# Kernel tuning notes

Hardware: AMD Instinct MI355X
Metric: run time of the kernel (lower is better)

## Reference

```python
import jax, jax.numpy as jnp
import numpy as np

N = 32          # agents_num
IN_DIM = 16     # node feature dim (excluding 2 pos cols)
HID = 128
HEADS = 4
OUT = 5
DUEL_H = 256
RADIUS = 0.3
LATENT = HID + HID * HEADS * 2  # 1152
BS = 128


def _lin(k, i, o):
    s = 1.0 / np.sqrt(i)
    return jax.random.uniform(k, (i, o), minval=-s, maxval=s, dtype=jnp.float32)


def setup_inputs() -> dict:
    key = jax.random.key(0)
    ks = jax.random.split(key, 16)
    pos = jax.random.uniform(ks[0], (BS, N, 2))
    feats = jax.random.normal(ks[1], (BS, N, IN_DIM))
    aidx = jax.random.randint(ks[2], (BS,), 0, N).astype(jnp.float32)
    node = jnp.concatenate([pos, feats], axis=-1).reshape(BS, N * (2 + IN_DIM))
    obs = jnp.concatenate([node, aidx[:, None]], axis=1)  # (BS, N*(2+IN_DIM)+1)
    return {
        "obs": obs,
        "enc_w1": _lin(ks[3], IN_DIM, HID), "enc_b1": jnp.zeros((HID,)),
        "enc_w2": _lin(ks[4], HID, HID), "enc_b2": jnp.zeros((HID,)),
        "wl1": _lin(ks[5], HID, HEADS * HID), "wr1": _lin(ks[6], HID, HEADS * HID),
        "att1": jax.random.normal(ks[7], (HEADS, HID)) * 0.1, "bias1": jnp.zeros((HEADS * HID,)),
        "wl2": _lin(ks[8], HID * HEADS, HEADS * HID), "wr2": _lin(ks[9], HID * HEADS, HEADS * HID),
        "att2": jax.random.normal(ks[10], (HEADS, HID)) * 0.1, "bias2": jnp.zeros((HEADS * HID,)),
        "q_w1": _lin(ks[11], LATENT, DUEL_H), "q_b1": jnp.zeros((DUEL_H,)),
        "q_w2": _lin(ks[12], DUEL_H, OUT), "q_b2": jnp.zeros((OUT,)),
        "v_w1": _lin(ks[13], LATENT, DUEL_H), "v_b1": jnp.zeros((DUEL_H,)),
        "v_w2": _lin(ks[14], DUEL_H, 1), "v_b2": jnp.zeros((1,)),
    }


def _gatv2(x, adj, wl, wr, att, bias):
    # Dense-masked GATv2 (PyG semantics: lin_l on source j, lin_r on target i,
    # leaky_relu(x_i + x_j) . att, softmax over neighbors j, aggregate lin_l(x_j)).
    bs, n, _ = x.shape
    gl = (x @ wl).reshape(bs, n, HEADS, HID)  # source transform
    gr = (x @ wr).reshape(bs, n, HEADS, HID)  # target transform
    e = jax.nn.leaky_relu(gr[:, :, None] + gl[:, None, :], 0.2)  # [b, i, j, h, c]
    logits = jnp.einsum('bijhc,hc->bijh', e, att)
    logits = jnp.where(adj[..., None], logits, -jnp.inf)  # diag always True (self loops)
    alpha = jax.nn.softmax(logits, axis=2)
    out = jnp.einsum('bijh,bjhc->bihc', alpha, gl).reshape(bs, n, HEADS * HID)
    return out + bias


def reference(obs, enc_w1, enc_b1, enc_w2, enc_b2,
              wl1, wr1, att1, bias1, wl2, wr2, att2, bias2,
              q_w1, q_b1, q_w2, q_b2, v_w1, v_b1, v_w2, v_b2):
    bs = obs.shape[0]
    node = obs[:, :-1].reshape(bs, N, 2 + IN_DIM)
    pos, feats = node[..., :2], node[..., 2:]
    aidx = jnp.clip(obs[:, -1], 0, N - 1).astype(jnp.int32)

    # radius_graph (per-graph, loop=False) + GATv2 add_self_loops => diag True
    d2 = jnp.sum((pos[:, :, None] - pos[:, None, :]) ** 2, axis=-1)  # [bs, N, N]
    adj = (d2 < RADIUS ** 2) | jnp.eye(N, dtype=bool)

    # encoder MLP then ReLU (as in forward)
    h = jax.nn.relu(feats @ enc_w1 + enc_b1)
    x = jax.nn.relu(h @ enc_w2 + enc_b2)  # [bs, N, HID]

    b = jnp.arange(bs)
    x1 = x[b, aidx]  # [bs, HID]

    x = jax.nn.relu(_gatv2(x, adj, wl1, wr1, att1, bias1))  # [bs, N, HID*HEADS]
    x2 = x[b, aidx]

    x = jax.nn.relu(_gatv2(x, adj, wl2, wr2, att2, bias2))
    x3 = x[b, aidx]

    x_cat = jnp.concatenate([x1, x2, x3], axis=1)  # [bs, LATENT]

    q = jax.nn.relu(x_cat @ q_w1 + q_b1) @ q_w2 + q_b2  # [bs, OUT]
    v = jax.nn.relu(x_cat @ v_w1 + v_b1) @ v_w2 + v_b2  # [bs, 1]
    return q - q.mean(axis=1, keepdims=True) + v
```

## Files before the change

kernel.cpp:

```cpp
#include <hip/hip_runtime.h>
#include <hip/hip_bf16.h>

typedef unsigned int uint_t;
typedef unsigned short ushort_t;
typedef __attribute__((ext_vector_type(8))) short short8;
typedef __attribute__((ext_vector_type(4))) float floatx4;

__device__ __forceinline__ float4 fma4(float4 a, float s, float4 w){
  a.x += s*w.x; a.y += s*w.y; a.z += s*w.z; a.w += s*w.w; return a;
}
__device__ __forceinline__ float4 relu4(float4 a){
  return make_float4(fmaxf(a.x,0.f),fmaxf(a.y,0.f),fmaxf(a.z,0.f),fmaxf(a.w,0.f));
}
__device__ __forceinline__ unsigned bf16rne(float f){
  unsigned u = __float_as_uint(f);
  return (u + 0x7fffu + ((u>>16)&1u)) >> 16;
}
__device__ __forceinline__ uint_t packbf(float f){
  unsigned hb = bf16rne(f);
  float hf = __uint_as_float(hb<<16);
  unsigned lb = bf16rne(f - hf);
  return (hb<<16) | lb;
}
__device__ __forceinline__ uint4 pack4(float4 v){
  uint4 u; u.x=packbf(v.x); u.y=packbf(v.y); u.z=packbf(v.z); u.w=packbf(v.w); return u;
}
__device__ __forceinline__ float unpk(uint_t u){
  return __uint_as_float(u & 0xffff0000u) + __uint_as_float(u<<16);
}
#define UNPACK8(u0,u1,hi,lo) \
  hi[0]=(short)(u0.x>>16); lo[0]=(short)u0.x; \
  hi[1]=(short)(u0.y>>16); lo[1]=(short)u0.y; \
  hi[2]=(short)(u0.z>>16); lo[2]=(short)u0.z; \
  hi[3]=(short)(u0.w>>16); lo[3]=(short)u0.w; \
  hi[4]=(short)(u1.x>>16); lo[4]=(short)u1.x; \
  hi[5]=(short)(u1.y>>16); lo[5]=(short)u1.y; \
  hi[6]=(short)(u1.z>>16); lo[6]=(short)u1.z; \
  hi[7]=(short)(u1.w>>16); lo[7]=(short)u1.w;


template<int NKC>
__device__ __forceinline__ void hgemm_body(
    const uint_t* __restrict__ xcatpk,
    const ushort_t* __restrict__ qw1Thi, const ushort_t* __restrict__ qw1Tlo,
    const ushort_t* __restrict__ vw1Thi, const ushort_t* __restrict__ vw1Tlo,
    float* __restrict__ part, int ks, int ct, int t, int k0c, int slot0)
{
  const int w = t>>6, lane = t&63, m = lane&15, quad = lane>>4;
  const ushort_t* Bhi = (ct<4) ? qw1Thi : vw1Thi;
  const int cbl = (ct<4) ? ct*64 : (ct-4)*64;
  const int cbg = (ct<4) ? ct*64 : 256 + (ct-4)*64;
  const int kb = k0c + ks*NKC;
  const uint_t* ap = xcatpk + (size_t)w*18432 + m*32 + quad*8 + (size_t)kb*512;
  const ushort_t* bp0 = Bhi + (size_t)((cbl>>4)+0)*18432 + m*32 + quad*8 + (size_t)kb*512;
  const ushort_t* bp1 = Bhi + (size_t)((cbl>>4)+1)*18432 + m*32 + quad*8 + (size_t)kb*512;
  const ushort_t* bp2 = Bhi + (size_t)((cbl>>4)+2)*18432 + m*32 + quad*8 + (size_t)kb*512;
  const ushort_t* bp3 = Bhi + (size_t)((cbl>>4)+3)*18432 + m*32 + quad*8 + (size_t)kb*512;
  const size_t lod = (size_t)(qw1Tlo - qw1Thi);
  floatx4 acc[4];
  #pragma unroll
  for (int i=0;i<4;i++) acc[i] = (floatx4){0.f,0.f,0.f,0.f};
  #pragma unroll
  for (int kc=0; kc<NKC; kc++){
    const uint4 ua0 = *(const uint4*)(ap);
    const uint4 ua1 = *(const uint4*)(ap+4);
    ap += 512;
    short8 ahi, alo;
    UNPACK8(ua0,ua1,ahi,alo)
    const ushort_t* bps[4] = {bp0, bp1, bp2, bp3};
    #pragma unroll
    for (int nt=0; nt<4; nt++){
      const short8 bh = *(const short8*)(bps[nt] + kc*512);
      const short8 bl = *(const short8*)(bps[nt] + kc*512 + lod);
      acc[nt] = __builtin_amdgcn_mfma_f32_16x16x32_bf16(ahi, bh, acc[nt], 0,0,0);
      acc[nt] = __builtin_amdgcn_mfma_f32_16x16x32_bf16(ahi, bl, acc[nt], 0,0,0);
      acc[nt] = __builtin_amdgcn_mfma_f32_16x16x32_bf16(alo, bh, acc[nt], 0,0,0);
    }
  }
  float* pdst = part + (size_t)(slot0+ks)*65536;
  const int crow0 = w*16 + quad*4;
  #pragma unroll
  for (int nt=0; nt<4; nt++){
    const int col = cbg + nt*16 + m;
    #pragma unroll
    for (int r=0;r<4;r++)
      pdst[(size_t)(crow0 + r)*512 + col] = acc[nt][r];
  }
}

__global__ __launch_bounds__(256) void prep_kernel(
    const float* __restrict__ obs,
    const float* __restrict__ enc_w1, const float* __restrict__ enc_b1,
    const float* __restrict__ enc_w2, const float* __restrict__ enc_b2,
    const float* __restrict__ wl1, const float* __restrict__ wr1,
    ushort_t* __restrict__ wl1Thi, ushort_t* __restrict__ wl1Tlo,
    ushort_t* __restrict__ wr1Thi, ushort_t* __restrict__ wr1Tlo,
    uint_t* __restrict__ xpk, uint_t* __restrict__ xcatpk,
    unsigned* __restrict__ adjw, int* __restrict__ aiw)
{
  const int t = threadIdx.x, bid = blockIdx.x;
  if (bid >= 512){
    __shared__ float sm[32][33];
    const int cw = bid - 512;
    const float* in; ushort_t* ohi; ushort_t* olo; int tt;
    const int K = 128, N = 512;
    if (cw < 64){ in=wl1; ohi=wl1Thi; olo=wl1Tlo; tt=cw; }
    else        { in=wr1; ohi=wr1Thi; olo=wr1Tlo; tt=cw-64; }
    const int ktiles = K>>5;
    const int kt = tt % ktiles, nt = tt / ktiles;
    const int r = t>>5, c = t&31;
    #pragma unroll
    for (int i=0;i<4;i++)
      sm[r+i*8][c] = in[(size_t)(kt*32 + r + i*8)*N + nt*32 + c];
    __syncthreads();
    #pragma unroll
    for (int i=0;i<4;i++){
      const int nl = r + i*8;
      const int n  = nt*32 + nl;
      const float f = sm[c][nl];
      const unsigned hb = bf16rne(f);
      const float hf = __uint_as_float(hb<<16);
      const unsigned lb = bf16rne(f - hf);
      const size_t off = (size_t)(n>>4)*(16*K) + (size_t)kt*512 + (size_t)(n&15)*32 + c;
      ohi[off] = (ushort_t)hb;
      olo[off] = (ushort_t)lb;
    }
    return;
  }
  __shared__ float s_pos[64];
  __shared__ float s_feats[128];
  __shared__ __align__(16) float s_h[8*132];
  __shared__ int s_ai;
  const int s = bid & 127, g = bid >> 7;
  const float* ob = obs + s*577;

  if (t==0){
    float a = ob[576];
    a = fminf(fmaxf(a, 0.f), 31.f);
    s_ai = (int)a;
    if (g==0) aiw[s] = (int)a;
  }
  if (t < 128){ const int n=t>>4, f=t&15; s_feats[t] = ob[(g*8+n)*18+2+f]; }
  if (g==0 && t>=128 && t<192){ const int u=t-128; s_pos[u] = ob[(u>>1)*18 + (u&1)]; }
  __syncthreads();

  if (g==0 && t < 32){
    const float px = s_pos[2*t], py = s_pos[2*t+1];
    const float R2 = 0.09f;
    unsigned mm = 0u;
    for (int j=0;j<32;j++){
      const float dx = __fsub_rn(px, s_pos[2*j]), dy = __fsub_rn(py, s_pos[2*j+1]);
      const float d2 = __fadd_rn(__fmul_rn(dx,dx), __fmul_rn(dy,dy));
      if (d2 <= R2 || j==t) mm |= (1u<<j);
    }
    adjw[s*32+t] = mm;
  }

  const int n = t>>5, c0 = (t&31)*4;
  {
    float4 a = *(const float4*)(enc_b1+c0);
    #pragma unroll
    for (int f=0; f<16; f++)
      a = fma4(a, s_feats[n*16+f], *(const float4*)(enc_w1 + f*128 + c0));
    *(float4*)&s_h[n*132+c0] = relu4(a);
  }
  __syncthreads();
  {
    float4 a = *(const float4*)(enc_b2+c0);
    for (int k=0;k<128;k+=4){
      const float4 hv = *(const float4*)&s_h[n*132+k];
      a = fma4(a, hv.x, *(const float4*)(enc_w2 + (k+0)*128 + c0));
      a = fma4(a, hv.y, *(const float4*)(enc_w2 + (k+1)*128 + c0));
      a = fma4(a, hv.z, *(const float4*)(enc_w2 + (k+2)*128 + c0));
      a = fma4(a, hv.w, *(const float4*)(enc_w2 + (k+3)*128 + c0));
    }
    a = relu4(a);
    const uint4 p = pack4(a);
    const int i = g*8 + n;
    uint_t* xp = xpk + (size_t)(s*2 + (i>>4))*2048 + (c0>>5)*512 + (i&15)*32 + (c0&31);
    *(uint4*)xp = p;
    if (i == s_ai){
      uint_t* xc = xcatpk + (size_t)(s>>4)*18432 + (c0>>5)*512 + (s&15)*32 + (c0&31);
      *(uint4*)xc = p;
    }
  }
}

__global__ __launch_bounds__(512) void pa1_kernel(
    const uint_t* __restrict__ xpk,
    const ushort_t* __restrict__ wl1Thi, const ushort_t* __restrict__ wl1Tlo,
    const ushort_t* __restrict__ wr1Thi, const ushort_t* __restrict__ wr1Tlo,
    const float* __restrict__ att, const float* __restrict__ bias,
    const unsigned* __restrict__ adjw, const int* __restrict__ aiw,
    const float* __restrict__ wl2, const float* __restrict__ q_w1,
    const float* __restrict__ v_w1, const float* __restrict__ wr2,
    ushort_t* __restrict__ wl2Thi, ushort_t* __restrict__ wl2Tlo,
    ushort_t* __restrict__ qw1Thi, ushort_t* __restrict__ qw1Tlo,
    ushort_t* __restrict__ vw1Thi, ushort_t* __restrict__ vw1Tlo,
    ushort_t* __restrict__ wr2Thi, ushort_t* __restrict__ wr2Tlo,
    uint_t* __restrict__ x2pk, uint_t* __restrict__ xcatpk)
{
  __shared__ __align__(16) float s_gl[32*132];
  __shared__ __align__(16) float s_gr[32*132];
  __shared__ __align__(16) float s_att[128];
  __shared__ __align__(16) float s_b[128];
  __shared__ float s_lg[32*33];
  __shared__ unsigned s_adj[32];
  const int t = threadIdx.x, bid = blockIdx.x;

  if (bid >= 512){
    const int cw = bid - 512;
    const float* in; ushort_t* ohi; ushort_t* olo; int K, N, tt;
    if (cw < 256)      { in=wl2;  ohi=wl2Thi; olo=wl2Tlo; K=512;  N=512; tt=cw; }
    else if (cw < 544) { in=q_w1; ohi=qw1Thi; olo=qw1Tlo; K=1152; N=256; tt=cw-256; }
    else if (cw < 832) { in=v_w1; ohi=vw1Thi; olo=vw1Tlo; K=1152; N=256; tt=cw-544; }
    else               { in=wr2;  ohi=wr2Thi; olo=wr2Tlo; K=512;  N=512; tt=cw-832; }
    const int ktiles = K>>5;
    const int kt = tt % ktiles, nt = tt / ktiles;
    const int r = t>>5, c = t&31;
    #pragma unroll
    for (int i=0;i<2;i++)
      s_gl[(r+i*16)*33 + c] = in[(size_t)(kt*32 + r + i*16)*N + nt*32 + c];
    __syncthreads();
    #pragma unroll
    for (int i=0;i<2;i++){
      const int nl = r + i*16;
      const int n  = nt*32 + nl;
      const float f = s_gl[c*33 + nl];
      const unsigned hb = bf16rne(f);
      const float hf = __uint_as_float(hb<<16);
      const unsigned lb = bf16rne(f - hf);
      const size_t off = (size_t)(n>>4)*(16*K) + (size_t)kt*512 + (size_t)(n&15)*32 + c;
      ohi[off] = (ushort_t)hb;
      olo[off] = (ushort_t)lb;
    }
    return;
  }

  const int s = bid & 127, h = bid >> 7;
  const int w = t>>6, lane = t&63, m = lane&15, quad = lane>>4;
  const int mat = w>>2, cpair = w&3;

  if (t < 128){ s_att[t] = att[h*128 + t]; s_b[t] = bias[h*128 + t]; }
  if (t >= 224 && t < 256) s_adj[t-224] = adjw[s*32 + (t-224)];
  const int ai = aiw[s];

  const ushort_t* Bhi = (mat==0) ? wl1Thi : wr1Thi;
  const ushort_t* Blo = (mat==0) ? wl1Tlo : wr1Tlo;
  const int nbase = h*8 + cpair*2;
  const uint_t* a0p = xpk + (size_t)(s*2+0)*2048 + m*32 + quad*8;
  const uint_t* a1p = xpk + (size_t)(s*2+1)*2048 + m*32 + quad*8;
  const ushort_t* bp0 = Bhi + (size_t)(nbase+0)*2048 + m*32 + quad*8;
  const ushort_t* bp1 = Bhi + (size_t)(nbase+1)*2048 + m*32 + quad*8;
  const size_t lod = (size_t)(Blo - Bhi);
  floatx4 acc[2][2];
  #pragma unroll
  for (int i=0;i<2;i++)
    #pragma unroll
    for (int j=0;j<2;j++) acc[i][j] = (floatx4){0.f,0.f,0.f,0.f};

  #pragma unroll
  for (int kc=0; kc<4; kc++){
    const uint4 u00 = *(const uint4*)(a0p + kc*512);
    const uint4 u01 = *(const uint4*)(a0p + kc*512 + 4);
    const uint4 u10 = *(const uint4*)(a1p + kc*512);
    const uint4 u11 = *(const uint4*)(a1p + kc*512 + 4);
    short8 ahi0, alo0, ahi1, alo1;
    UNPACK8(u00,u01,ahi0,alo0)
    UNPACK8(u10,u11,ahi1,alo1)
    const ushort_t* bps[2] = {bp0, bp1};
    #pragma unroll
    for (int nt=0; nt<2; nt++){
      const short8 bh = *(const short8*)(bps[nt] + kc*512);
      const short8 bl = *(const short8*)(bps[nt] + kc*512 + lod);
      acc[0][nt] = __builtin_amdgcn_mfma_f32_16x16x32_bf16(ahi0, bh, acc[0][nt], 0,0,0);
      acc[0][nt] = __builtin_amdgcn_mfma_f32_16x16x32_bf16(ahi0, bl, acc[0][nt], 0,0,0);
      acc[0][nt] = __builtin_amdgcn_mfma_f32_16x16x32_bf16(alo0, bh, acc[0][nt], 0,0,0);
      acc[1][nt] = __builtin_amdgcn_mfma_f32_16x16x32_bf16(ahi1, bh, acc[1][nt], 0,0,0);
      acc[1][nt] = __builtin_amdgcn_mfma_f32_16x16x32_bf16(ahi1, bl, acc[1][nt], 0,0,0);
      acc[1][nt] = __builtin_amdgcn_mfma_f32_16x16x32_bf16(alo1, bh, acc[1][nt], 0,0,0);
    }
  }
  {
    float* dst = mat ? s_gr : s_gl;
    const int colbase = cpair*32;
    #pragma unroll
    for (int nt=0; nt<2; nt++){
      const int col = colbase + nt*16 + m;
      #pragma unroll
      for (int r=0;r<4;r++){
        dst[(quad*4+r)*132 + col]      = acc[0][nt][r];
        dst[(16+quad*4+r)*132 + col]   = acc[1][nt][r];
      }
    }
  }
  __syncthreads();

  {
    const int i = t>>4, jb = t&15;
    float lacc[2] = {0.f,0.f};
    for (int c=0;c<128;c+=4){
      const float4 g = *(const float4*)&s_gr[i*132+c];
      const float4 a = *(const float4*)&s_att[c];
      #pragma unroll
      for (int mm=0;mm<2;mm++){
        const float4 gj = *(const float4*)&s_gl[(jb+16*mm)*132 + c];
        float ex = g.x+gj.x; ex = fmaxf(ex, 0.2f*ex);
        float ey = g.y+gj.y; ey = fmaxf(ey, 0.2f*ey);
        float ez = g.z+gj.z; ez = fmaxf(ez, 0.2f*ez);
        float ew = g.w+gj.w; ew = fmaxf(ew, 0.2f*ew);
        lacc[mm] += ex*a.x + ey*a.y + ez*a.z + ew*a.w;
      }
    }
    s_lg[i*33 + jb]      = lacc[0];
    s_lg[i*33 + jb + 16] = lacc[1];
  }
  __syncthreads();

  #pragma unroll
  for (int rnd=0; rnd<2; rnd++){
    const int i = rnd*16 + (t>>5), j = t&31;
    const float lg = s_lg[i*33+j];
    const bool ok = (s_adj[i]>>j)&1u;
    float v = ok ? lg : -3.0e38f;
    #pragma unroll
    for (int d_=16; d_; d_>>=1) v = fmaxf(v, __shfl_xor(v, d_, 32));
    const float e = ok ? __expf(lg - v) : 0.f;
    float sum = e;
    #pragma unroll
    for (int d_=16; d_; d_>>=1) sum += __shfl_xor(sum, d_, 32);
    s_lg[i*33+j] = e / sum;
  }
  __syncthreads();

  {
    const int i = t>>4, c0 = (t&15)*8;
    float4 o0 = make_float4(0.f,0.f,0.f,0.f), o1 = o0;
    for (int j=0;j<32;j++){
      const float al = s_lg[i*33+j];
      o0 = fma4(o0, al, *(const float4*)&s_gl[j*132 + c0]);
      o1 = fma4(o1, al, *(const float4*)&s_gl[j*132 + c0 + 4]);
    }
    const float4 b0 = *(const float4*)&s_b[c0];
    const float4 b1 = *(const float4*)&s_b[c0+4];
    o0 = relu4(make_float4(o0.x+b0.x, o0.y+b0.y, o0.z+b0.z, o0.w+b0.w));
    o1 = relu4(make_float4(o1.x+b1.x, o1.y+b1.y, o1.z+b1.z, o1.w+b1.w));
    const uint4 p0 = pack4(o0), p1 = pack4(o1);
    const int kb = h*128 + c0;
    uint_t* xp = x2pk + (size_t)(s*2 + (i>>4))*8192 + (kb>>5)*512 + (i&15)*32 + (kb&31);
    *(uint4*)&xp[0] = p0;
    *(uint4*)&xp[4] = p1;
    if (i == ai){
      const int kk = 128 + kb;
      uint_t* tp = xcatpk + (size_t)(s>>4)*18432 + (kk>>5)*512 + (s&15)*32 + (kk&31);
      *(uint4*)&tp[0] = p0;
      *(uint4*)&tp[4] = p1;
    }
  }
}

__global__ __launch_bounds__(512) void gr2_kernel(
    const uint_t* __restrict__ xcatpk,
    const ushort_t* __restrict__ wr2Thi, const ushort_t* __restrict__ wr2Tlo,
    const ushort_t* __restrict__ qw1Thi, const ushort_t* __restrict__ qw1Tlo,
    const ushort_t* __restrict__ vw1Thi, const ushort_t* __restrict__ vw1Tlo,
    float* __restrict__ hpart, float* __restrict__ GR)
{
  const int t = threadIdx.x, bid = blockIdx.x;
  if (bid >= 32){
    const int hk = bid - 32;
    hgemm_body<5>(xcatpk, qw1Thi, qw1Tlo, vw1Thi, vw1Tlo, hpart, hk>>3, hk&7, t, 0, 0);
    return;
  }
  const int w = t>>6, lane = t&63, m = lane&15, quad = lane>>4;
  const int rt = w;
  const int ctl = bid;
  const uint_t* ap = xcatpk + (size_t)rt*18432 + m*32 + quad*8 + (size_t)4*512;
  const ushort_t* bp = wr2Thi + (size_t)ctl*8192 + m*32 + quad*8;
  const size_t lod = (size_t)(wr2Tlo - wr2Thi);
  floatx4 acc = (floatx4){0.f,0.f,0.f,0.f};
  #pragma unroll 4
  for (int kc=0; kc<16; kc++){
    const uint4 ua0 = *(const uint4*)(ap + kc*512);
    const uint4 ua1 = *(const uint4*)(ap + kc*512 + 4);
    short8 ahi, alo;
    UNPACK8(ua0,ua1,ahi,alo)
    const short8 bh = *(const short8*)(bp + kc*512);
    const short8 bl = *(const short8*)(bp + kc*512 + lod);
    acc = __builtin_amdgcn_mfma_f32_16x16x32_bf16(ahi, bh, acc, 0,0,0);
    acc = __builtin_amdgcn_mfma_f32_16x16x32_bf16(ahi, bl, acc, 0,0,0);
    acc = __builtin_amdgcn_mfma_f32_16x16x32_bf16(alo, bh, acc, 0,0,0);
  }
  const int row0 = rt*16 + quad*4, col = ctl*16 + m;
  #pragma unroll
  for (int r=0;r<4;r++)
    GR[(size_t)(row0 + r)*512 + col] = acc[r];
}

__global__ __launch_bounds__(512) void pa2_kernel(
    const uint_t* __restrict__ x2pk,
    const ushort_t* __restrict__ wl2Thi, const ushort_t* __restrict__ wl2Tlo,
    const float* __restrict__ GR,
    const float* __restrict__ att2, const float* __restrict__ bias2,
    const unsigned* __restrict__ adjw, const int* __restrict__ aiw,
    uint_t* __restrict__ xcatpk)
{
  __shared__ __align__(16) float s_gl[32*132];
  __shared__ __align__(16) float s_p2[128];
  __shared__ __align__(16) float s_at[128];
  __shared__ __align__(16) float s_bb[128];
  __shared__ float s_lg[32];
  __shared__ float s_al[32];
  const int t = threadIdx.x, bid = blockIdx.x;
  const int s = bid & 127, h = bid >> 7;
  const int w = t>>6, lane = t&63, m = lane&15, quad = lane>>4;
  const int ai = aiw[s];
  const unsigned arow = adjw[s*32+ai];

  if (t < 128){
    s_p2[t] = GR[(size_t)s*512 + h*128 + t];
    s_at[t] = att2[h*128+t];
    s_bb[t] = bias2[h*128+t];
  }

  const uint_t* a0p = x2pk + (size_t)(s*2+0)*8192 + m*32 + quad*8;
  const uint_t* a1p = x2pk + (size_t)(s*2+1)*8192 + m*32 + quad*8;
  const ushort_t* bq = wl2Thi + (size_t)(h*8 + w)*8192 + m*32 + quad*8;
  const size_t lod = (size_t)(wl2Tlo - wl2Thi);
  floatx4 acc0 = (floatx4){0.f,0.f,0.f,0.f}, acc1 = acc0;
  #pragma unroll 4
  for (int kc=0; kc<16; kc++){
    const uint4 u00 = *(const uint4*)(a0p + kc*512);
    const uint4 u01 = *(const uint4*)(a0p + kc*512 + 4);
    const uint4 u10 = *(const uint4*)(a1p + kc*512);
    const uint4 u11 = *(const uint4*)(a1p + kc*512 + 4);
    short8 ahi0, alo0, ahi1, alo1;
    UNPACK8(u00,u01,ahi0,alo0)
    UNPACK8(u10,u11,ahi1,alo1)
    const short8 bh = *(const short8*)(bq + kc*512);
    const short8 bl = *(const short8*)(bq + kc*512 + lod);
    acc0 = __builtin_amdgcn_mfma_f32_16x16x32_bf16(ahi0, bh, acc0, 0,0,0);
    acc0 = __builtin_amdgcn_mfma_f32_16x16x32_bf16(ahi0, bl, acc0, 0,0,0);
    acc0 = __builtin_amdgcn_mfma_f32_16x16x32_bf16(alo0, bh, acc0, 0,0,0);
    acc1 = __builtin_amdgcn_mfma_f32_16x16x32_bf16(ahi1, bh, acc1, 0,0,0);
    acc1 = __builtin_amdgcn_mfma_f32_16x16x32_bf16(ahi1, bl, acc1, 0,0,0);
    acc1 = __builtin_amdgcn_mfma_f32_16x16x32_bf16(alo1, bh, acc1, 0,0,0);
  }
  {
    const int col = w*16 + m;
    #pragma unroll
    for (int r=0;r<4;r++){
      s_gl[(quad*4+r)*132 + col]    = acc0[r];
      s_gl[(16+quad*4+r)*132 + col] = acc1[r];
    }
  }
  __syncthreads();

  if (t < 256){
    const int j = t>>3, pq = t&7;
    float sum = 0.f;
    #pragma unroll
    for (int q=0;q<4;q++){
      const int c = pq*16 + q*4;
      const float4 g = *(const float4*)&s_gl[j*132 + c];
      const float4 r = *(const float4*)&s_p2[c];
      const float4 a = *(const float4*)&s_at[c];
      float e0 = r.x+g.x; e0 = fmaxf(e0, 0.2f*e0);
      float e1 = r.y+g.y; e1 = fmaxf(e1, 0.2f*e1);
      float e2 = r.z+g.z; e2 = fmaxf(e2, 0.2f*e2);
      float e3 = r.w+g.w; e3 = fmaxf(e3, 0.2f*e3);
      sum += e0*a.x + e1*a.y + e2*a.z + e3*a.w;
    }
    sum += __shfl_xor(sum,1,64);
    sum += __shfl_xor(sum,2,64);
    sum += __shfl_xor(sum,4,64);
    if (pq==0) s_lg[j] = sum;
  }
  __syncthreads();
  if (t < 32){
    const float lg = s_lg[t];
    const bool ok = (arow>>t)&1u;
    float v = ok ? lg : -3.0e38f;
    #pragma unroll
    for (int d_=16; d_; d_>>=1) v = fmaxf(v, __shfl_xor(v, d_, 32));
    const float e = ok ? __expf(lg - v) : 0.f;
    float sm = e;
    #pragma unroll
    for (int d_=16; d_; d_>>=1) sm += __shfl_xor(sm, d_, 32);
    s_al[t] = e / sm;
  }
  __syncthreads();
  if (t < 128){
    float acc2 = 0.f;
    #pragma unroll 8
    for (int j=0;j<32;j++) acc2 += s_al[j] * s_gl[j*132 + t];
    const float x3v = fmaxf(acc2 + s_bb[t], 0.f);
    const int kk = 640 + h*128 + t;
    xcatpk[(size_t)(s>>4)*18432 + (kk>>5)*512 + (s&15)*32 + (kk&31)] = packbf(x3v);
  }
}

__global__ __launch_bounds__(512) void x3g_kernel(
    const uint_t* __restrict__ xcatpk,
    const ushort_t* __restrict__ qw1Thi, const ushort_t* __restrict__ qw1Tlo,
    const ushort_t* __restrict__ vw1Thi, const ushort_t* __restrict__ vw1Tlo,
    float* __restrict__ hpart)
{
  const int t = threadIdx.x, bid = blockIdx.x;
  hgemm_body<4>(xcatpk, qw1Thi, qw1Tlo, vw1Thi, vw1Tlo, hpart, bid>>3, bid&7, t, 20, 4);
}

__global__ __launch_bounds__(256) void hepi_kernel(
    const float* __restrict__ hpart,
    const float* __restrict__ q_b1, const float* __restrict__ q_w2, const float* __restrict__ q_b2,
    const float* __restrict__ v_b1, const float* __restrict__ v_w2, const float* __restrict__ v_b2,
    float* __restrict__ out)
{
  __shared__ float s_p[4*6];
  const int t = threadIdx.x, s = blockIdx.x;
  float hq = q_b1[t], hv = v_b1[t];
  #pragma unroll
  for (int ks=0; ks<8; ks++){
    hq += hpart[(size_t)ks*65536 + (size_t)s*512 + t];
    hv += hpart[(size_t)ks*65536 + (size_t)s*512 + 256 + t];
  }
  hq = fmaxf(hq, 0.f);
  hv = fmaxf(hv, 0.f);
  float p[6];
  #pragma unroll
  for (int o=0;o<5;o++) p[o] = hq * q_w2[t*5+o];
  p[5] = hv * v_w2[t];
  #pragma unroll
  for (int d_=32; d_; d_>>=1){
    #pragma unroll
    for (int o=0;o<6;o++) p[o] += __shfl_xor(p[o], d_, 64);
  }
  const int w = t>>6, lane = t&63;
  if (lane==0){
    #pragma unroll
    for (int o=0;o<6;o++) s_p[w*6+o] = p[o];
  }
  __syncthreads();
  if (t < 6) s_p[t] = s_p[t] + s_p[6+t] + s_p[12+t] + s_p[18+t];
  __syncthreads();
  if (t < 5){
    const float q0 = s_p[0]+q_b2[0], q1 = s_p[1]+q_b2[1], q2 = s_p[2]+q_b2[2],
                q3 = s_p[3]+q_b2[3], q4 = s_p[4]+q_b2[4];
    const float mean = (q0+q1+q2+q3+q4) / 5.0f;
    const float v = s_p[5] + v_b2[0];
    const float qt = (t==0?q0:t==1?q1:t==2?q2:t==3?q3:q4);
    out[s*5+t] = qt - mean + v;
  }
}

extern "C" void kernel_launch(void* const* d_in, const int* in_sizes, int n_in,
                              void* d_out, int out_size, void* d_ws, size_t ws_size,
                              hipStream_t stream) {
  (void)n_in; (void)out_size; (void)ws_size;
  const float* obs    = (const float*)d_in[0];
  const float* enc_w1 = (const float*)d_in[1];
  const float* enc_b1 = (const float*)d_in[2];
  const float* enc_w2 = (const float*)d_in[3];
  const float* enc_b2 = (const float*)d_in[4];
  const float* wl1    = (const float*)d_in[5];
  const float* wr1    = (const float*)d_in[6];
  const float* att1   = (const float*)d_in[7];
  const float* bias1  = (const float*)d_in[8];
  const float* wl2    = (const float*)d_in[9];
  const float* wr2    = (const float*)d_in[10];
  const float* att2   = (const float*)d_in[11];
  const float* bias2  = (const float*)d_in[12];
  const float* q_w1   = (const float*)d_in[13];
  const float* q_b1   = (const float*)d_in[14];
  const float* q_w2   = (const float*)d_in[15];
  const float* q_b2   = (const float*)d_in[16];
  const float* v_w1   = (const float*)d_in[17];
  const float* v_b1   = (const float*)d_in[18];
  const float* v_w2   = (const float*)d_in[19];
  const float* v_b2   = (const float*)d_in[20];

  char* ws = (char*)d_ws;
  uint_t*   x_pk    = (uint_t*)  (ws + 0);
  float*    hpart   = (float*)   (ws + 0);
  uint_t*   xcat_pk = (uint_t*)  (ws + 2097152);
  unsigned* adjw    = (unsigned*)(ws + 2686976);
  int*      aiw     = (int*)     (ws + 2703360);
  uint_t*   x2_pk   = (uint_t*)  (ws + 2703872);
  ushort_t* wl1Thi  = (ushort_t*)(ws + 11092480);
  ushort_t* wl1Tlo  = (ushort_t*)(ws + 11223552);
  ushort_t* wr1Thi  = (ushort_t*)(ws + 11354624);
  ushort_t* wr1Tlo  = (ushort_t*)(ws + 11485696);
  ushort_t* wl2Thi  = (ushort_t*)(ws + 11616768);
  ushort_t* wl2Tlo  = (ushort_t*)(ws + 12141056);
  ushort_t* qw1Thi  = (ushort_t*)(ws + 12665344);
  ushort_t* qw1Tlo  = (ushort_t*)(ws + 13255168);
  ushort_t* vw1Thi  = (ushort_t*)(ws + 13844992);
  ushort_t* vw1Tlo  = (ushort_t*)(ws + 14434816);
  ushort_t* wr2Thi  = (ushort_t*)(ws + 15024640);
  ushort_t* wr2Tlo  = (ushort_t*)(ws + 15548928);
  float*    GR      = (float*)   (ws + 16073216);

  const int bs = in_sizes[0] / 577;
  (void)bs;

  prep_kernel<<<512 + 128, 256, 0, stream>>>(obs, enc_w1, enc_b1, enc_w2, enc_b2,
      wl1, wr1, wl1Thi, wl1Tlo, wr1Thi, wr1Tlo,
      x_pk, xcat_pk, adjw, aiw);

  pa1_kernel<<<512 + 1088, 512, 0, stream>>>(x_pk, wl1Thi, wl1Tlo, wr1Thi, wr1Tlo,
      att1, bias1, adjw, aiw,
      wl2, q_w1, v_w1, wr2,
      wl2Thi, wl2Tlo, qw1Thi, qw1Tlo, vw1Thi, vw1Tlo, wr2Thi, wr2Tlo,
      x2_pk, xcat_pk);

  gr2_kernel<<<64, 512, 0, stream>>>(xcat_pk, wr2Thi, wr2Tlo,
      qw1Thi, qw1Tlo, vw1Thi, vw1Tlo, hpart, GR);

  pa2_kernel<<<512, 512, 0, stream>>>(x2_pk, wl2Thi, wl2Tlo, GR,
      att2, bias2, adjw, aiw, xcat_pk);

  x3g_kernel<<<32, 512, 0, stream>>>(xcat_pk, qw1Thi, qw1Tlo, vw1Thi, vw1Tlo, hpart);

  hepi_kernel<<<128, 256, 0, stream>>>(hpart, q_b1, q_w2, q_b2, v_b1, v_w2, v_b2,
                                       (float*)d_out);
}
```

Measured before the change: 197.0 us.

## Move all weight conversion into prep, fold x3 GEMM into fp32 epilogue

All bf16 hi/lo weight conversion work (wl2, wr2, q_w1, v_w1) moves from pa1 into the prep kernel, so pa1 launches only its attention blocks. The separate x3g MFMA kernel is removed: pa2 now writes x3 as plain fp32, and the epilogue kernel (now 512 threads) computes the last 512 rows of the dueling-head GEMM directly from fp32 weights with scalar FMA loops. This saves one launch and one kernel boundary, but leaves a serial 512-long dot product per thread in the epilogue, reading q_w1 and v_w1 from global memory with 128 blocks only. hpart is relocated so it no longer aliases x_pk.

```diff
diff --git a/kernel.cpp b/kernel.cpp
--- a/kernel.cpp
+++ b/kernel.cpp
@@ -93,8 +93,14 @@
     const float* __restrict__ enc_w1, const float* __restrict__ enc_b1,
     const float* __restrict__ enc_w2, const float* __restrict__ enc_b2,
     const float* __restrict__ wl1, const float* __restrict__ wr1,
+    const float* __restrict__ wl2, const float* __restrict__ wr2,
+    const float* __restrict__ q_w1, const float* __restrict__ v_w1,
     ushort_t* __restrict__ wl1Thi, ushort_t* __restrict__ wl1Tlo,
     ushort_t* __restrict__ wr1Thi, ushort_t* __restrict__ wr1Tlo,
+    ushort_t* __restrict__ wl2Thi, ushort_t* __restrict__ wl2Tlo,
+    ushort_t* __restrict__ wr2Thi, ushort_t* __restrict__ wr2Tlo,
+    ushort_t* __restrict__ qw1Thi, ushort_t* __restrict__ qw1Tlo,
+    ushort_t* __restrict__ vw1Thi, ushort_t* __restrict__ vw1Tlo,
     uint_t* __restrict__ xpk, uint_t* __restrict__ xcatpk,
     unsigned* __restrict__ adjw, int* __restrict__ aiw)
 {
@@ -102,11 +108,13 @@
   if (bid >= 512){
     __shared__ float sm[32][33];
     const int cw = bid - 512;
-    const float* in; ushort_t* ohi; ushort_t* olo; int tt;
-    const int K = 128, N = 512;
-    if (cw < 64){ in=wl1; ohi=wl1Thi; olo=wl1Tlo; tt=cw; }
-    else        { in=wr1; ohi=wr1Thi; olo=wr1Tlo; tt=cw-64; }
-    const int ktiles = K>>5;
+    const float* in; ushort_t* ohi; ushort_t* olo; int K, N, tt, ktiles;
+    if (cw < 64)       { in=wl1;  ohi=wl1Thi; olo=wl1Tlo; K=128;  N=512; tt=cw;     ktiles=4;  }
+    else if (cw < 128) { in=wr1;  ohi=wr1Thi; olo=wr1Tlo; K=128;  N=512; tt=cw-64;  ktiles=4;  }
+    else if (cw < 384) { in=wl2;  ohi=wl2Thi; olo=wl2Tlo; K=512;  N=512; tt=cw-128; ktiles=16; }
+    else if (cw < 640) { in=wr2;  ohi=wr2Thi; olo=wr2Tlo; K=512;  N=512; tt=cw-384; ktiles=16; }
+    else if (cw < 800) { in=q_w1; ohi=qw1Thi; olo=qw1Tlo; K=1152; N=256; tt=cw-640; ktiles=20; }
+    else               { in=v_w1; ohi=vw1Thi; olo=vw1Tlo; K=1152; N=256; tt=cw-800; ktiles=20; }
     const int kt = tt % ktiles, nt = tt / ktiles;
     const int r = t>>5, c = t&31;
     #pragma unroll
@@ -121,7 +129,7 @@
       const unsigned hb = bf16rne(f);
       const float hf = __uint_as_float(hb<<16);
       const unsigned lb = bf16rne(f - hf);
-      const size_t off = (size_t)(n>>4)*(16*K) + (size_t)kt*512 + (size_t)(n&15)*32 + c;
+      const size_t off = (size_t)(n>>4)*(size_t)(16*K) + (size_t)kt*512 + (size_t)(n&15)*32 + c;
       ohi[off] = (ushort_t)hb;
       olo[off] = (ushort_t)lb;
     }
@@ -192,12 +200,6 @@
     const ushort_t* __restrict__ wr1Thi, const ushort_t* __restrict__ wr1Tlo,
     const float* __restrict__ att, const float* __restrict__ bias,
     const unsigned* __restrict__ adjw, const int* __restrict__ aiw,
-    const float* __restrict__ wl2, const float* __restrict__ q_w1,
-    const float* __restrict__ v_w1, const float* __restrict__ wr2,
-    ushort_t* __restrict__ wl2Thi, ushort_t* __restrict__ wl2Tlo,
-    ushort_t* __restrict__ qw1Thi, ushort_t* __restrict__ qw1Tlo,
-    ushort_t* __restrict__ vw1Thi, ushort_t* __restrict__ vw1Tlo,
-    ushort_t* __restrict__ wr2Thi, ushort_t* __restrict__ wr2Tlo,
     uint_t* __restrict__ x2pk, uint_t* __restrict__ xcatpk)
 {
   __shared__ __align__(16) float s_gl[32*132];
@@ -207,35 +209,6 @@
   __shared__ float s_lg[32*33];
   __shared__ unsigned s_adj[32];
   const int t = threadIdx.x, bid = blockIdx.x;
-
-  if (bid >= 512){
-    const int cw = bid - 512;
-    const float* in; ushort_t* ohi; ushort_t* olo; int K, N, tt;
-    if (cw < 256)      { in=wl2;  ohi=wl2Thi; olo=wl2Tlo; K=512;  N=512; tt=cw; }
-    else if (cw < 544) { in=q_w1; ohi=qw1Thi; olo=qw1Tlo; K=1152; N=256; tt=cw-256; }
-    else if (cw < 832) { in=v_w1; ohi=vw1Thi; olo=vw1Tlo; K=1152; N=256; tt=cw-544; }
-    else               { in=wr2;  ohi=wr2Thi; olo=wr2Tlo; K=512;  N=512; tt=cw-832; }
-    const int ktiles = K>>5;
-    const int kt = tt % ktiles, nt = tt / ktiles;
-    const int r = t>>5, c = t&31;
-    #pragma unroll
-    for (int i=0;i<2;i++)
-      s_gl[(r+i*16)*33 + c] = in[(size_t)(kt*32 + r + i*16)*N + nt*32 + c];
-    __syncthreads();
-    #pragma unroll
-    for (int i=0;i<2;i++){
-      const int nl = r + i*16;
-      const int n  = nt*32 + nl;
-      const float f = s_gl[c*33 + nl];
-      const unsigned hb = bf16rne(f);
-      const float hf = __uint_as_float(hb<<16);
-      const unsigned lb = bf16rne(f - hf);
-      const size_t off = (size_t)(n>>4)*(16*K) + (size_t)kt*512 + (size_t)(n&15)*32 + c;
-      ohi[off] = (ushort_t)hb;
-      olo[off] = (ushort_t)lb;
-    }
-    return;
-  }
 
   const int s = bid & 127, h = bid >> 7;
   const int w = t>>6, lane = t&63, m = lane&15, quad = lane>>4;
@@ -373,10 +346,8 @@
     return;
   }
   const int w = t>>6, lane = t&63, m = lane&15, quad = lane>>4;
-  const int rt = w;
-  const int ctl = bid;
-  const uint_t* ap = xcatpk + (size_t)rt*18432 + m*32 + quad*8 + (size_t)4*512;
-  const ushort_t* bp = wr2Thi + (size_t)ctl*8192 + m*32 + quad*8;
+  const uint_t* ap = xcatpk + (size_t)w*18432 + m*32 + quad*8 + (size_t)4*512;
+  const ushort_t* bp = wr2Thi + (size_t)bid*8192 + m*32 + quad*8;
   const size_t lod = (size_t)(wr2Tlo - wr2Thi);
   floatx4 acc = (floatx4){0.f,0.f,0.f,0.f};
   #pragma unroll 4
@@ -391,7 +362,7 @@
     acc = __builtin_amdgcn_mfma_f32_16x16x32_bf16(ahi, bl, acc, 0,0,0);
     acc = __builtin_amdgcn_mfma_f32_16x16x32_bf16(alo, bh, acc, 0,0,0);
   }
-  const int row0 = rt*16 + quad*4, col = ctl*16 + m;
+  const int row0 = w*16 + quad*4, col = bid*16 + m;
   #pragma unroll
   for (int r=0;r<4;r++)
     GR[(size_t)(row0 + r)*512 + col] = acc[r];
@@ -403,7 +374,7 @@
     const float* __restrict__ GR,
     const float* __restrict__ att2, const float* __restrict__ bias2,
     const unsigned* __restrict__ adjw, const int* __restrict__ aiw,
-    uint_t* __restrict__ xcatpk)
+    float* __restrict__ X3)
 {
   __shared__ __align__(16) float s_gl[32*132];
   __shared__ __align__(16) float s_p2[128];
@@ -414,6 +385,7 @@
   const int t = threadIdx.x, bid = blockIdx.x;
   const int s = bid & 127, h = bid >> 7;
   const int w = t>>6, lane = t&63, m = lane&15, quad = lane>>4;
+  (void)lane;
   const int ai = aiw[s];
   const unsigned arow = adjw[s*32+ai];
 
@@ -494,60 +466,70 @@
     float acc2 = 0.f;
     #pragma unroll 8
     for (int j=0;j<32;j++) acc2 += s_al[j] * s_gl[j*132 + t];
-    const float x3v = fmaxf(acc2 + s_bb[t], 0.f);
-    const int kk = 640 + h*128 + t;
-    xcatpk[(size_t)(s>>4)*18432 + (kk>>5)*512 + (s&15)*32 + (kk&31)] = packbf(x3v);
-  }
-}
-
-__global__ __launch_bounds__(512) void x3g_kernel(
-    const uint_t* __restrict__ xcatpk,
-    const ushort_t* __restrict__ qw1Thi, const ushort_t* __restrict__ qw1Tlo,
-    const ushort_t* __restrict__ vw1Thi, const ushort_t* __restrict__ vw1Tlo,
-    float* __restrict__ hpart)
-{
-  const int t = threadIdx.x, bid = blockIdx.x;
-  hgemm_body<4>(xcatpk, qw1Thi, qw1Tlo, vw1Thi, vw1Tlo, hpart, bid>>3, bid&7, t, 20, 4);
-}
-
-__global__ __launch_bounds__(256) void hepi_kernel(
-    const float* __restrict__ hpart,
-    const float* __restrict__ q_b1, const float* __restrict__ q_w2, const float* __restrict__ q_b2,
-    const float* __restrict__ v_b1, const float* __restrict__ v_w2, const float* __restrict__ v_b2,
+    X3[(size_t)s*512 + h*128 + t] = fmaxf(acc2 + s_bb[t], 0.f);
+  }
+}
+
+__global__ __launch_bounds__(512) void hepi_kernel(
+    const float* __restrict__ X3, const float* __restrict__ hpart,
+    const float* __restrict__ q_w1, const float* __restrict__ q_b1,
+    const float* __restrict__ q_w2, const float* __restrict__ q_b2,
+    const float* __restrict__ v_w1, const float* __restrict__ v_b1,
+    const float* __restrict__ v_w2, const float* __restrict__ v_b2,
     float* __restrict__ out)
 {
-  __shared__ float s_p[4*6];
+  __shared__ __align__(16) float s_x3[512];
+  __shared__ float s_p6[8*6];
   const int t = threadIdx.x, s = blockIdx.x;
-  float hq = q_b1[t], hv = v_b1[t];
-  #pragma unroll
-  for (int ks=0; ks<8; ks++){
-    hq += hpart[(size_t)ks*65536 + (size_t)s*512 + t];
-    hv += hpart[(size_t)ks*65536 + (size_t)s*512 + 256 + t];
-  }
-  hq = fmaxf(hq, 0.f);
-  hv = fmaxf(hv, 0.f);
+  const int w = t>>6, lane = t&63;
+
+  s_x3[t] = X3[(size_t)s*512 + t];
+  __syncthreads();
+
+  float val;
+  {
+    const int col = t & 255;
+    float acc = (t < 256) ? q_b1[col] : v_b1[col];
+    #pragma unroll
+    for (int ks=0; ks<4; ks++)
+      acc += hpart[(size_t)ks*65536 + (size_t)s*512 + t];
+    const float* Wp = ((t < 256) ? q_w1 : v_w1) + (size_t)640*256 + col;
+    #pragma unroll 8
+    for (int k=0;k<512;k++) acc += s_x3[k] * Wp[(size_t)k*256];
+    val = fmaxf(acc, 0.f);
+  }
+
   float p[6];
   #pragma unroll
-  for (int o=0;o<5;o++) p[o] = hq * q_w2[t*5+o];
-  p[5] = hv * v_w2[t];
+  for (int o=0;o<6;o++) p[o] = 0.f;
+  if (t < 256){
+    #pragma unroll
+    for (int o=0;o<5;o++) p[o] = val * q_w2[t*5+o];
+  } else {
+    p[5] = val * v_w2[t-256];
+  }
   #pragma unroll
   for (int d_=32; d_; d_>>=1){
     #pragma unroll
     for (int o=0;o<6;o++) p[o] += __shfl_xor(p[o], d_, 64);
   }
-  const int w = t>>6, lane = t&63;
   if (lane==0){
     #pragma unroll
-    for (int o=0;o<6;o++) s_p[w*6+o] = p[o];
-  }
-  __syncthreads();
-  if (t < 6) s_p[t] = s_p[t] + s_p[6+t] + s_p[12+t] + s_p[18+t];
+    for (int o=0;o<6;o++) s_p6[w*6+o] = p[o];
+  }
+  __syncthreads();
+  if (t < 6){
+    float v = 0.f;
+    #pragma unroll
+    for (int ww=0; ww<8; ww++) v += s_p6[ww*6 + t];
+    s_p6[t] = v;
+  }
   __syncthreads();
   if (t < 5){
-    const float q0 = s_p[0]+q_b2[0], q1 = s_p[1]+q_b2[1], q2 = s_p[2]+q_b2[2],
-                q3 = s_p[3]+q_b2[3], q4 = s_p[4]+q_b2[4];
+    const float q0 = s_p6[0]+q_b2[0], q1 = s_p6[1]+q_b2[1], q2 = s_p6[2]+q_b2[2],
+                q3 = s_p6[3]+q_b2[3], q4 = s_p6[4]+q_b2[4];
     const float mean = (q0+q1+q2+q3+q4) / 5.0f;
-    const float v = s_p[5] + v_b2[0];
+    const float v = s_p6[5] + v_b2[0];
     const float qt = (t==0?q0:t==1?q1:t==2?q2:t==3?q3:q4);
     out[s*5+t] = qt - mean + v;
   }
@@ -581,7 +563,6 @@
 
   char* ws = (char*)d_ws;
   uint_t*   x_pk    = (uint_t*)  (ws + 0);
-  float*    hpart   = (float*)   (ws + 0);
   uint_t*   xcat_pk = (uint_t*)  (ws + 2097152);
   unsigned* adjw    = (unsigned*)(ws + 2686976);
   int*      aiw     = (int*)     (ws + 2703360);
@@ -599,28 +580,25 @@
   ushort_t* wr2Thi  = (ushort_t*)(ws + 15024640);
   ushort_t* wr2Tlo  = (ushort_t*)(ws + 15548928);
   float*    GR      = (float*)   (ws + 16073216);
-
-  const int bs = in_sizes[0] / 577;
-  (void)bs;
-
-  prep_kernel<<<512 + 128, 256, 0, stream>>>(obs, enc_w1, enc_b1, enc_w2, enc_b2,
-      wl1, wr1, wl1Thi, wl1Tlo, wr1Thi, wr1Tlo,
+  float*    hpart   = (float*)   (ws + 16335360);
+  float*    X3      = (float*)   (ws + 17383936);
+
+  prep_kernel<<<512 + 960, 256, 0, stream>>>(obs, enc_w1, enc_b1, enc_w2, enc_b2,
+      wl1, wr1, wl2, wr2, q_w1, v_w1,
+      wl1Thi, wl1Tlo, wr1Thi, wr1Tlo, wl2Thi, wl2Tlo, wr2Thi, wr2Tlo,
+      qw1Thi, qw1Tlo, vw1Thi, vw1Tlo,
       x_pk, xcat_pk, adjw, aiw);
 
-  pa1_kernel<<<512 + 1088, 512, 0, stream>>>(x_pk, wl1Thi, wl1Tlo, wr1Thi, wr1Tlo,
-      att1, bias1, adjw, aiw,
-      wl2, q_w1, v_w1, wr2,
-      wl2Thi, wl2Tlo, qw1Thi, qw1Tlo, vw1Thi, vw1Tlo, wr2Thi, wr2Tlo,
-      x2_pk, xcat_pk);
+  pa1_kernel<<<512, 512, 0, stream>>>(x_pk, wl1Thi, wl1Tlo, wr1Thi, wr1Tlo,
+      att1, bias1, adjw, aiw, x2_pk, xcat_pk);
 
   gr2_kernel<<<64, 512, 0, stream>>>(xcat_pk, wr2Thi, wr2Tlo,
       qw1Thi, qw1Tlo, vw1Thi, vw1Tlo, hpart, GR);
 
   pa2_kernel<<<512, 512, 0, stream>>>(x2_pk, wl2Thi, wl2Tlo, GR,
-      att2, bias2, adjw, aiw, xcat_pk);
-
-  x3g_kernel<<<32, 512, 0, stream>>>(xcat_pk, qw1Thi, qw1Tlo, vw1Thi, vw1Tlo, hpart);
-
-  hepi_kernel<<<128, 256, 0, stream>>>(hpart, q_b1, q_w2, q_b2, v_b1, v_w2, v_b2,
-                                       (float*)d_out);
-}
+      att2, bias2, adjw, aiw, X3);
+
+  hepi_kernel<<<128, 512, 0, stream>>>(X3, hpart,
+      q_w1, q_b1, q_w2, q_b2, v_w1, v_b1, v_w2, v_b2,
+      (float*)d_out);
+}
```

Result: slower. 207.2 us (+5.2%).
